# Optimization experiments

Measured on AMD Instinct MI355X. Metric: run time of the kernel, lower is better.

Reference implementation:

```python
import jax, jax.numpy as jnp
import numpy as np

B, SE, SD, IN_DIM, D, DEPTH, H, DH, M, FF, NBINS = 8, 2048, 1024, 1280, 512, 4, 8, 64, 266, 2048, 128

def _ln(x, g, b):
    mu = x.mean(-1, keepdims=True)
    var = ((x - mu) ** 2).mean(-1, keepdims=True)
    return (x - mu) / jnp.sqrt(var + 1e-5) * g + b

def _gelu(x):
    return jax.nn.gelu(x, approximate=False)

def _sinusoidal(x, dim):
    # sinusoidal embedding of integer expression bins -> [.., dim]
    half = dim // 2
    freqs = jnp.exp(-jnp.log(10000.0) * jnp.arange(half, dtype=jnp.float32) / half)
    ang = x[..., None].astype(jnp.float32) * freqs
    return jnp.concatenate([jnp.sin(ang), jnp.cos(ang)], axis=-1)

def _split_heads(x):
    b, s, _ = x.shape
    return x.reshape(b, s, H, DH).transpose(0, 2, 1, 3)

def _merge_heads(x):
    b, h, s, d = x.shape
    return x.transpose(0, 2, 1, 3).reshape(b, s, h * d)

def _favor_attention(q, k, v, proj):
    # FAVOR+ softmax-kernel linear attention (non-causal), performer-style
    dn = DH ** -0.25
    ratio = M ** -0.5
    eps = 1e-4
    qd = jnp.einsum('bhsd,md->bhsm', q * dn, proj)
    kd = jnp.einsum('bhsd,md->bhsm', k * dn, proj)
    q_diag = 0.5 * (q ** 2).sum(-1, keepdims=True) * dn * dn
    k_diag = 0.5 * (k ** 2).sum(-1, keepdims=True) * dn * dn
    qp = ratio * (jnp.exp(qd - q_diag - jnp.max(qd, axis=-1, keepdims=True)) + eps)
    kp = ratio * (jnp.exp(kd - k_diag - jnp.max(kd)) + eps)
    k_sum = kp.sum(axis=2)                                   # [b,h,m]
    d_inv = 1.0 / jnp.einsum('bhsm,bhm->bhs', qp, k_sum)     # [b,h,s]
    kv = jnp.einsum('bhsm,bhsd->bhmd', kp, v)                # [b,h,m,d]
    return jnp.einsum('bhsm,bhmd->bhsd', qp, kv) * d_inv[..., None]

def _forward(var_input_encoder, var_input_decoder, var_W, var_b, enc_ln_g, enc_ln_b, dec_ln_g, dec_ln_b, p_ln1_g, p_ln1_b, p_Wq, p_Wk, p_Wv, p_Wo, p_bo, p_ln2_g, p_ln2_b, p_w1, p_b1, p_w2, p_b2, proj, ca_Wq, ca_Wk, ca_Wv, ca_Wo, ca_bo, cross_ln_g, cross_ln_b, ffd_w1, ffd_b1, ffd_w2, ffd_b2, out_ln_g, out_ln_b, head_W, head_b, expression_encoder):
    expr = _sinusoidal(expression_encoder, D)            # [B,SE,D]
    enc = var_input_encoder @ var_W + var_b              # [B,SE,D]
    dec = var_input_decoder @ var_W + var_b              # [B,SD,D]
    x = _ln(enc + expr, enc_ln_g, enc_ln_b)
    # Performer encoder: pre-LN self-attn (FAVOR+) + pre-LN FF, residuals
    for i in range(DEPTH):
        y = _ln(x, p_ln1_g[i], p_ln1_b[i])
        q = _split_heads(y @ p_Wq[i])
        k = _split_heads(y @ p_Wk[i])
        v = _split_heads(y @ p_Wv[i])
        x = x + (_merge_heads(_favor_attention(q, k, v, proj[i])) @ p_Wo[i] + p_bo[i])
        y = _ln(x, p_ln2_g[i], p_ln2_b[i])
        x = x + (_gelu(y @ p_w1[i] + p_b1[i]) @ p_w2[i] + p_b2[i])
    context = x
    # decoder: LN -> softmax cross-attention over encoder context
    dec = _ln(dec, dec_ln_g, dec_ln_b)
    q = _split_heads(dec @ ca_Wq)
    k = _split_heads(context @ ca_Wk)
    v = _split_heads(context @ ca_Wv)
    scores = jnp.einsum('bhqd,bhkd->bhqk', q, k) * (DH ** -0.5)
    o = _merge_heads(jnp.einsum('bhqk,bhkd->bhqd', jax.nn.softmax(scores, axis=-1), v)) @ ca_Wo + ca_bo
    out = _ln(o + dec, cross_ln_g, cross_ln_b)
    out = _gelu(out @ ffd_w1 + ffd_b1) @ ffd_w2 + ffd_b2   # note: no residual around FF (as in source)
    out = _ln(out, out_ln_g, out_ln_b)
    return out @ head_W + head_b                            # [B,SD,NBINS]

def setup_inputs() -> dict:
    key = jax.random.key(0)
    ks = iter(jax.random.split(key, 64))
    def w(shape, scale=0.02):
        return jax.random.normal(next(ks), shape, dtype=jnp.float32) * scale
    inp = {
        'var_input_encoder': jax.random.normal(next(ks), (B, SE, IN_DIM), dtype=jnp.float32),
        'var_input_decoder': jax.random.normal(next(ks), (B, SD, IN_DIM), dtype=jnp.float32),
        'expression_encoder': jax.random.randint(next(ks), (B, SE), 0, NBINS, dtype=jnp.int32),
        'var_W': w((IN_DIM, D)), 'var_b': jnp.zeros((D,), jnp.float32),
        'enc_ln_g': jnp.ones((D,), jnp.float32), 'enc_ln_b': jnp.zeros((D,), jnp.float32),
        'dec_ln_g': jnp.ones((D,), jnp.float32), 'dec_ln_b': jnp.zeros((D,), jnp.float32),
        'p_ln1_g': jnp.ones((DEPTH, D), jnp.float32), 'p_ln1_b': jnp.zeros((DEPTH, D), jnp.float32),
        'p_Wq': w((DEPTH, D, H * DH)), 'p_Wk': w((DEPTH, D, H * DH)), 'p_Wv': w((DEPTH, D, H * DH)),
        'p_Wo': w((DEPTH, H * DH, D)), 'p_bo': jnp.zeros((DEPTH, D), jnp.float32),
        'p_ln2_g': jnp.ones((DEPTH, D), jnp.float32), 'p_ln2_b': jnp.zeros((DEPTH, D), jnp.float32),
        'p_w1': w((DEPTH, D, FF)), 'p_b1': jnp.zeros((DEPTH, FF), jnp.float32),
        'p_w2': w((DEPTH, FF, D)), 'p_b2': jnp.zeros((DEPTH, D), jnp.float32),
        'proj': jax.random.normal(next(ks), (DEPTH, M, DH), dtype=jnp.float32),
        'ca_Wq': w((D, H * DH)), 'ca_Wk': w((D, H * DH)), 'ca_Wv': w((D, H * DH)),
        'ca_Wo': w((H * DH, D)), 'ca_bo': jnp.zeros((D,), jnp.float32),
        'cross_ln_g': jnp.ones((D,), jnp.float32), 'cross_ln_b': jnp.zeros((D,), jnp.float32),
        'ffd_w1': w((D, FF)), 'ffd_b1': jnp.zeros((FF,), jnp.float32),
        'ffd_w2': w((FF, D)), 'ffd_b2': jnp.zeros((D,), jnp.float32),
        'out_ln_g': jnp.ones((D,), jnp.float32), 'out_ln_b': jnp.zeros((D,), jnp.float32),
        'head_W': w((D, NBINS)), 'head_b': jnp.zeros((NBINS,), jnp.float32),
    }
    return inp

def reference(var_input_encoder, var_input_decoder, expression_encoder, var_W, var_b, enc_ln_g, enc_ln_b, dec_ln_g, dec_ln_b, p_ln1_g, p_ln1_b, p_Wq, p_Wk, p_Wv, p_Wo, p_bo, p_ln2_g, p_ln2_b, p_w1, p_b1, p_w2, p_b2, proj, ca_Wq, ca_Wk, ca_Wv, ca_Wo, ca_bo, cross_ln_g, cross_ln_b, ffd_w1, ffd_b1, ffd_w2, ffd_b2, out_ln_g, out_ln_b, head_W, head_b):
    return _forward(var_input_encoder, var_input_decoder, var_W, var_b, enc_ln_g, enc_ln_b, dec_ln_g, dec_ln_b, p_ln1_g, p_ln1_b, p_Wq, p_Wk, p_Wv, p_Wo, p_bo, p_ln2_g, p_ln2_b, p_w1, p_b1, p_w2, p_b2, proj, ca_Wq, ca_Wk, ca_Wv, ca_Wo, ca_bo, cross_ln_g, cross_ln_b, ffd_w1, ffd_b1, ffd_w2, ffd_b2, out_ln_g, out_ln_b, head_W, head_b, expression_encoder)
```

## Files before the change

### kernel.cpp

```cpp
#include <hip/hip_runtime.h>
#include <hip/hip_bf16.h>
#include <math.h>

constexpr int cB = 8, cSE = 2048, cSD = 1024, cIN = 1280, cD = 512,
              cDEPTH = 4, cH = 8, cDH = 64, cM = 266, cFF = 2048, cNB = 128;
constexpr int cMP = 288;

#define DEV __device__ __forceinline__

typedef __bf16 bf16;
typedef __attribute__((ext_vector_type(8))) __bf16 bf16x8;
typedef __attribute__((ext_vector_type(4))) __bf16 bf16x4;
typedef __attribute__((ext_vector_type(2))) __bf16 bf16x2;
typedef __attribute__((ext_vector_type(4))) float f32x4;

DEV float gelu_f(float x) { return 0.5f * x * (1.0f + erff(x * 0.70710678118654752440f)); }

DEV float wave_sum(float v) {
#pragma unroll
  for (int o = 32; o; o >>= 1) v += __shfl_xor(v, o);
  return v;
}
DEV float wave_max(float v) {
#pragma unroll
  for (int o = 32; o; o >>= 1) v = fmaxf(v, __shfl_xor(v, o));
  return v;
}

#define GL2LDS(gp, lp) __builtin_amdgcn_global_load_lds(                    \
    (const __attribute__((address_space(1))) void*)(gp),                    \
    (__attribute__((address_space(3))) void*)(lp), 16, 0, 0)

template <int OUT, int ACT, bool BIAS, bool RES>
__global__ __launch_bounds__(256) void gemm_mfma(
    const bf16* __restrict__ A, const bf16* __restrict__ Bt,
    void* __restrict__ Cv, bf16* __restrict__ Cv2,
    const float* __restrict__ bias, int M, int N, int K) {
  __shared__ bf16 As[128 * 32];
  __shared__ bf16 Bs[128 * 32];
  const int t = threadIdx.x, l = t & 63, w = t >> 6;
  const int g = l >> 4, c = l & 15;
  const int nwg = gridDim.x * gridDim.y;
  int id = blockIdx.y * gridDim.x + blockIdx.x;
  if ((nwg & 7) == 0) id = (id & 7) * (nwg >> 3) + (id >> 3);
  const int m0 = (id / gridDim.x) * 128, n0 = (id % gridDim.x) * 128;
  const int wr = (w >> 1) * 64, wc = (w & 1) * 64;
  const int srow = w * 32 + (l >> 2);
  const int scol = (l & 3) * 8;
  const bf16* gA = A + (size_t)(m0 + srow) * K + scol;
  const bf16* gB = Bt + (size_t)(n0 + srow) * K + scol;
  bf16* lA = As + w * 1024;
  bf16* lB = Bs + w * 1024;

  const f32x4 zero4 = {0.f, 0.f, 0.f, 0.f};
  f32x4 acc[4][4];
#pragma unroll
  for (int i = 0; i < 4; i++)
#pragma unroll
    for (int j = 0; j < 4; j++) acc[i][j] = zero4;

  for (int k0 = 0; k0 < K; k0 += 32) {
    GL2LDS(gA + k0, lA);
    GL2LDS(gA + (size_t)16 * K + k0, lA + 512);
    GL2LDS(gB + k0, lB);
    GL2LDS(gB + (size_t)16 * K + k0, lB + 512);
    __syncthreads();
    bf16x8 af[4], bfr[4];
#pragma unroll
    for (int i = 0; i < 4; i++)
      af[i] = *(const bf16x8*)(As + (wr + i * 16 + c) * 32 + g * 8);
#pragma unroll
    for (int j = 0; j < 4; j++)
      bfr[j] = *(const bf16x8*)(Bs + (wc + j * 16 + c) * 32 + g * 8);
#pragma unroll
    for (int i = 0; i < 4; i++)
#pragma unroll
      for (int j = 0; j < 4; j++)
        acc[i][j] = __builtin_amdgcn_mfma_f32_16x16x32_bf16(af[i], bfr[j], acc[i][j], 0, 0, 0);
    __syncthreads();
  }
  float* Cf = (float*)Cv;
  bf16* Cb = (bf16*)Cv;
#pragma unroll
  for (int i = 0; i < 4; i++) {
    const int mb = m0 + wr + i * 16 + g * 4;
#pragma unroll
    for (int j = 0; j < 4; j++) {
      const int n = n0 + wc + j * 16 + c;
      const float bv = BIAS ? bias[n] : 0.f;
#pragma unroll
      for (int r = 0; r < 4; r++) {
        float v = acc[i][j][r] + bv;
        if (ACT == 1) v = gelu_f(v);
        if (ACT == 2) v *= 0.18033688011112042f;
        const size_t idx = (size_t)(mb + r) * N + n;
        if (OUT == 0 || OUT == 2) {
          float* cp = Cf + idx;
          if (RES) v += *cp;
          *cp = v;
          if (OUT == 2) Cv2[idx] = (bf16)v;
        } else {
          Cb[idx] = (bf16)v;
        }
      }
    }
  }
}

__global__ __launch_bounds__(256) void mega_prep(
    const float* __restrict__ Wq, const float* __restrict__ Wk,
    const float* __restrict__ Wv, const float* __restrict__ Wo,
    const float* __restrict__ w1, const float* __restrict__ w2,
    const float* __restrict__ var_W, const float* __restrict__ proj,
    bf16* __restrict__ WL, bf16* __restrict__ WtVar,
    bf16* __restrict__ projB4) {
  const int z = blockIdx.y, bid = blockIdx.x, t = threadIdx.x;
  if (z == 25) {
    const int idx = bid * 256 + t;
    if (idx < 4 * cMP * cDH) {
      const int layer = idx / (cMP * cDH), r = idx % (cMP * cDH);
      const int m = r >> 6;
      projB4[idx] = (bf16)(m < cM ? proj[(size_t)layer * cM * cDH + r] * 0.35355339059327373f : 0.f);
    }
    return;
  }
  __shared__ float tile[32][33];
  const float* W;
  bf16* dst;
  int K, N;
  if (z == 24) {
    W = var_W; dst = WtVar; K = 1280; N = 512;
  } else {
    const int layer = z / 6, mat = z % 6;
    bf16* base = WL + (size_t)layer * 3145728;
    if (mat < 4) {
      W = (mat == 0 ? Wq : mat == 1 ? Wk : mat == 2 ? Wv : Wo) + (size_t)layer * 262144;
      dst = base + mat * 262144; K = 512; N = 512;
    } else if (mat == 4) {
      W = w1 + (size_t)layer * 1048576; dst = base + 1048576; K = 512; N = 2048;
    } else {
      W = w2 + (size_t)layer * 1048576; dst = base + 2097152; K = 2048; N = 512;
    }
  }
  const int nt = N >> 5;
  if (bid >= nt * (K >> 5)) return;
  const int n0 = (bid % nt) * 32, k0 = (bid / nt) * 32;
  const int tx = t & 31, ty = t >> 5;
#pragma unroll
  for (int i = ty; i < 32; i += 8) tile[i][tx] = W[(size_t)(k0 + i) * N + n0 + tx];
  __syncthreads();
#pragma unroll
  for (int i = ty; i < 32; i += 8)
    dst[(size_t)(n0 + i) * K + k0 + tx] = (bf16)tile[tx][i];
}

__global__ __launch_bounds__(256) void mega_prep_dec(
    const float* __restrict__ caWq, const float* __restrict__ caWk,
    const float* __restrict__ caWv, const float* __restrict__ caWo,
    const float* __restrict__ fw1, const float* __restrict__ fw2,
    const float* __restrict__ hW, bf16* __restrict__ WD) {
  const int z = blockIdx.y, bid = blockIdx.x, t = threadIdx.x;
  __shared__ float tile[32][33];
  const float* W;
  bf16* dst;
  int K, N;
  if (z < 4) {
    W = (z == 0 ? caWq : z == 1 ? caWk : z == 2 ? caWv : caWo);
    dst = WD + z * 262144; K = 512; N = 512;
  } else if (z == 4) {
    W = fw1; dst = WD + 1048576; K = 512; N = 2048;
  } else if (z == 5) {
    W = fw2; dst = WD + 2097152; K = 2048; N = 512;
  } else {
    W = hW; dst = WD + 3145728; K = 512; N = 128;
  }
  const int nt = N >> 5;
  if (bid >= nt * (K >> 5)) return;
  const int n0 = (bid % nt) * 32, k0 = (bid / nt) * 32;
  const int tx = t & 31, ty = t >> 5;
#pragma unroll
  for (int i = ty; i < 32; i += 8) tile[i][tx] = W[(size_t)(k0 + i) * N + n0 + tx];
  __syncthreads();
#pragma unroll
  for (int i = ty; i < 32; i += 8)
    dst[(size_t)(n0 + i) * K + k0 + tx] = (bf16)tile[tx][i];
}

__global__ __launch_bounds__(256) void castf2b(
    const float* __restrict__ x, bf16* __restrict__ y, int n) {
  int i = (blockIdx.x * 256 + threadIdx.x) * 4;
  const int stride = gridDim.x * 1024;
  for (; i < n; i += stride) {
    float4 v = *(const float4*)(x + i);
    bf16x4 o;
    o[0] = (bf16)v.x; o[1] = (bf16)v.y; o[2] = (bf16)v.z; o[3] = (bf16)v.w;
    *(bf16x4*)(y + i) = o;
  }
}

__global__ __launch_bounds__(256) void vtrans(
    const bf16* __restrict__ Vh, int ld, bf16* __restrict__ Vt) {
  __shared__ bf16 tile[64][65];
  const int z = blockIdx.y, b = z >> 3, h = z & 7;
  const int s0 = blockIdx.x * 64;
  const int t = threadIdx.x;
#pragma unroll
  for (int r = t >> 3; r < 64; r += 32) {
    bf16x8 v = *(const bf16x8*)(Vh + ((size_t)b * cSE + s0 + r) * ld + h * cDH + (t & 7) * 8);
#pragma unroll
    for (int e = 0; e < 8; e++) tile[(t & 7) * 8 + e][r] = v[e];
  }
  __syncthreads();
  bf16* vz = Vt + (size_t)z * 80 * cSE;
#pragma unroll
  for (int d = t >> 3; d < 64; d += 32) {
    bf16x8 o;
#pragma unroll
    for (int e = 0; e < 8; e++) o[e] = tile[d][(t & 7) * 8 + e];
    *(bf16x8*)(vz + (size_t)d * cSE + s0 + (t & 7) * 8) = o;
  }
  const int rr = t >> 4, seg = (t & 15) * 4;
  bf16x4 ov;
  const float val = (rr == 0) ? 1.f : 0.f;
  ov[0] = (bf16)val; ov[1] = (bf16)val; ov[2] = (bf16)val; ov[3] = (bf16)val;
  *(bf16x4*)(vz + (size_t)(64 + rr) * cSE + s0 + seg) = ov;
}

__global__ __launch_bounds__(256, 1) void favor_kmax(
    const bf16* __restrict__ Kh, int ld, const bf16* __restrict__ projB,
    float* __restrict__ bmax) {
  __shared__ float sm[4];
  const int z = blockIdx.y, b = z >> 3, h = z & 7;
  const int s0 = blockIdx.x * 128;
  const int t = threadIdx.x, l = t & 63, w = t >> 6, g = l >> 4, c = l & 15;
  const int wr = (w >> 1) * 64, wcol = (w & 1) * 144;
  const f32x4 zero4 = {0.f, 0.f, 0.f, 0.f};
  f32x4 acc[4][9];
#pragma unroll
  for (int i = 0; i < 4; i++)
#pragma unroll
    for (int j = 0; j < 9; j++) acc[i][j] = zero4;
  const size_t abase = ((size_t)b * cSE + s0) * ld + h * cDH;
#pragma unroll
  for (int k0 = 0; k0 < 64; k0 += 32) {
    bf16x8 af[4];
#pragma unroll
    for (int i = 0; i < 4; i++)
      af[i] = *(const bf16x8*)(Kh + abase + (size_t)(wr + i * 16 + c) * ld + k0 + g * 8);
#pragma unroll
    for (int j = 0; j < 9; j++) {
      bf16x8 bfr = *(const bf16x8*)(projB + (wcol + j * 16 + c) * 64 + k0 + g * 8);
#pragma unroll
      for (int i = 0; i < 4; i++)
        acc[i][j] = __builtin_amdgcn_mfma_f32_16x16x32_bf16(af[i], bfr, acc[i][j], 0, 0, 0);
    }
  }
  float m = -3e38f;
#pragma unroll
  for (int i = 0; i < 4; i++)
#pragma unroll
    for (int j = 0; j < 9; j++) {
      const int mc = wcol + j * 16 + c;
      if (mc < cM) {
#pragma unroll
        for (int r = 0; r < 4; r++) m = fmaxf(m, acc[i][j][r]);
      }
    }
  m = wave_max(m);
  if (l == 0) sm[w] = m;
  __syncthreads();
  if (t == 0)
    bmax[blockIdx.y * 16 + blockIdx.x] =
        fmaxf(fmaxf(sm[0], sm[1]), fmaxf(sm[2], sm[3]));
}

__global__ __launch_bounds__(256, 1) void favor_kkv(
    const bf16* __restrict__ Kh, int ld, const bf16* __restrict__ projB,
    const bf16* __restrict__ Vt, const float* __restrict__ bmax,
    float* __restrict__ part) {
  __shared__ bf16 kp[288 * 72];
  __shared__ float sm[4];
  const int z = blockIdx.y, b = z >> 3, h = z & 7;
  const int chunk = blockIdx.x;
  const int t = threadIdx.x, l = t & 63, w = t >> 6, g = l >> 4, c = l & 15;
  float gm;
  {
    float m = -1e30f;
    for (int i = t; i < 1024; i += 256) m = fmaxf(m, bmax[i]);
    m = wave_max(m);
    if (l == 0) sm[w] = m;
    __syncthreads();
    gm = fmaxf(fmaxf(sm[0], sm[1]), fmaxf(sm[2], sm[3]));
  }
  const int pr = (w >> 1) * 32;
  const int wcol = (w & 1) * 144;
  const int wm = (w & 1) * 144, wd = (w >> 1) * 32;
  const bool dden = (wd == 32);
  const float ratio = 0.061313927f;
  const f32x4 zero4 = {0.f, 0.f, 0.f, 0.f};
  f32x4 kacc[9][2], kaccx[9];
#pragma unroll
  for (int j = 0; j < 9; j++) {
    kacc[j][0] = zero4; kacc[j][1] = zero4; kaccx[j] = zero4;
  }
  const size_t kbase = (size_t)b * cSE * ld + h * cDH;
  const size_t vtz = (size_t)z * 80 * cSE;

  for (int st = 0; st < 256; st += 64) {
    const int sg = chunk * 256 + st;
    f32x4 pacc[2][9];
#pragma unroll
    for (int i = 0; i < 2; i++)
#pragma unroll
      for (int j = 0; j < 9; j++) pacc[i][j] = zero4;
    float sq[2] = {0.f, 0.f};
#pragma unroll
    for (int k0 = 0; k0 < 64; k0 += 32) {
      bf16x8 af[2];
#pragma unroll
      for (int i = 0; i < 2; i++) {
        af[i] = *(const bf16x8*)(Kh + kbase + (size_t)(sg + pr + i * 16 + c) * ld + k0 + g * 8);
#pragma unroll
        for (int e = 0; e < 8; e++) {
          const float v = (float)af[i][e];
          sq[i] += v * v;
        }
      }
#pragma unroll
      for (int j = 0; j < 9; j++) {
        bf16x8 bfr = *(const bf16x8*)(projB + (wcol + j * 16 + c) * 64 + k0 + g * 8);
        pacc[0][j] = __builtin_amdgcn_mfma_f32_16x16x32_bf16(af[0], bfr, pacc[0][j], 0, 0, 0);
        pacc[1][j] = __builtin_amdgcn_mfma_f32_16x16x32_bf16(af[1], bfr, pacc[1][j], 0, 0, 0);
      }
    }
#pragma unroll
    for (int i = 0; i < 2; i++) {
      sq[i] += __shfl_xor(sq[i], 16);
      sq[i] += __shfl_xor(sq[i], 32);
    }
    float rowsub[2][4];
#pragma unroll
    for (int i = 0; i < 2; i++)
#pragma unroll
      for (int r = 0; r < 4; r++)
        rowsub[i][r] = gm + 0.0625f * __shfl(sq[i], g * 4 + r);
    __syncthreads();
#pragma unroll
    for (int i = 0; i < 2; i++)
#pragma unroll
      for (int j = 0; j < 9; j++) {
        const int mc = wcol + j * 16 + c;
        bf16x4 o;
#pragma unroll
        for (int r = 0; r < 4; r++) {
          const float v = (mc < cM)
              ? ratio * (__expf(pacc[i][j][r] - rowsub[i][r]) + 1e-4f) : 0.f;
          o[r] = (bf16)v;
        }
        *(bf16x4*)(kp + (size_t)mc * 72 + pr + i * 16 + g * 4) = o;
      }
    __syncthreads();
#pragma unroll
    for (int k0 = 0; k0 < 64; k0 += 32) {
      bf16x8 bv0 = *(const bf16x8*)(Vt + vtz + (size_t)(wd + c) * cSE + sg + k0 + g * 8);
      bf16x8 bv1 = *(const bf16x8*)(Vt + vtz + (size_t)(wd + 16 + c) * cSE + sg + k0 + g * 8);
      bf16x8 bvx;
      if (dden)
        bvx = *(const bf16x8*)(Vt + vtz + (size_t)(64 + c) * cSE + sg + k0 + g * 8);
#pragma unroll
      for (int j = 0; j < 9; j++) {
        bf16x8 am = *(const bf16x8*)(kp + (size_t)(wm + j * 16 + c) * 72 + k0 + g * 8);
        kacc[j][0] = __builtin_amdgcn_mfma_f32_16x16x32_bf16(am, bv0, kacc[j][0], 0, 0, 0);
        kacc[j][1] = __builtin_amdgcn_mfma_f32_16x16x32_bf16(am, bv1, kacc[j][1], 0, 0, 0);
        if (dden)
          kaccx[j] = __builtin_amdgcn_mfma_f32_16x16x32_bf16(am, bvx, kaccx[j], 0, 0, 0);
      }
    }
  }
  float* po = part + ((size_t)z * 8 + chunk) * (cMP * 80);
#pragma unroll
  for (int j = 0; j < 9; j++)
#pragma unroll
    for (int i = 0; i < 2; i++)
#pragma unroll
      for (int r = 0; r < 4; r++)
        po[(size_t)(wm + j * 16 + g * 4 + r) * 80 + wd + i * 16 + c] = kacc[j][i][r];
  if (dden) {
#pragma unroll
    for (int j = 0; j < 9; j++)
#pragma unroll
      for (int r = 0; r < 4; r++)
        po[(size_t)(wm + j * 16 + g * 4 + r) * 80 + 64 + c] = kaccx[j][r];
  }
}

__global__ __launch_bounds__(256) void kv_reduce(
    const float* __restrict__ part, bf16* __restrict__ kvT) {
  const int z = blockIdx.y, q = blockIdx.x;
  const float* p = part + (size_t)z * 8 * (cMP * 80);
  bf16* o = kvT + (size_t)z * 80 * cMP;
  const int lo = q * 5760, hi = lo + 5760;
  for (int idx = lo + threadIdx.x; idx < hi; idx += 256) {
    const int m = idx / 80, d = idx - m * 80;
    float s = 0.f;
#pragma unroll
    for (int cc = 0; cc < 8; cc++) s += p[idx + (size_t)cc * (cMP * 80)];
    o[(size_t)d * cMP + m] = (bf16)s;
  }
}

__global__ __launch_bounds__(256, 1) void favor_qout(
    const bf16* __restrict__ Qh, int ld, const bf16* __restrict__ projB,
    const bf16* __restrict__ kvT, bf16* __restrict__ Y) {
  __shared__ bf16 Plds[128 * 296];
  __shared__ float rmaxs[4][64];
  __shared__ float denl[128];
  const int z = blockIdx.y, b = z >> 3, h = z & 7;
  const int s0 = blockIdx.x * 128;
  const int t = threadIdx.x, l = t & 63, w = t >> 6, g = l >> 4, c = l & 15;
  const int wr = (w >> 1) * 64, wcol = (w & 1) * 144;
  const f32x4 zero4 = {0.f, 0.f, 0.f, 0.f};
  f32x4 acc[4][9];
#pragma unroll
  for (int i = 0; i < 4; i++)
#pragma unroll
    for (int j = 0; j < 9; j++) acc[i][j] = zero4;
  float sq[4] = {0.f, 0.f, 0.f, 0.f};
  const size_t abase = ((size_t)b * cSE + s0) * ld + h * cDH;
#pragma unroll
  for (int k0 = 0; k0 < 64; k0 += 32) {
    bf16x8 af[4];
#pragma unroll
    for (int i = 0; i < 4; i++) {
      af[i] = *(const bf16x8*)(Qh + abase + (size_t)(wr + i * 16 + c) * ld + k0 + g * 8);
#pragma unroll
      for (int e = 0; e < 8; e++) {
        const float v = (float)af[i][e];
        sq[i] += v * v;
      }
    }
#pragma unroll
    for (int j = 0; j < 9; j++) {
      bf16x8 bfr = *(const bf16x8*)(projB + (wcol + j * 16 + c) * 64 + k0 + g * 8);
#pragma unroll
      for (int i = 0; i < 4; i++)
        acc[i][j] = __builtin_amdgcn_mfma_f32_16x16x32_bf16(af[i], bfr, acc[i][j], 0, 0, 0);
    }
  }
#pragma unroll
  for (int i = 0; i < 4; i++) {
    sq[i] += __shfl_xor(sq[i], 16);
    sq[i] += __shfl_xor(sq[i], 32);
  }
  const float ratio = 0.061313927f;
  float rowsub[4][4];
#pragma unroll
  for (int i = 0; i < 4; i++)
#pragma unroll
    for (int r = 0; r < 4; r++) {
      float m = -3e38f;
#pragma unroll
      for (int j = 0; j < 9; j++) {
        const int mc = wcol + j * 16 + c;
        m = (mc < cM) ? fmaxf(m, acc[i][j][r]) : m;
      }
      m = fmaxf(m, __shfl_xor(m, 1));
      m = fmaxf(m, __shfl_xor(m, 2));
      m = fmaxf(m, __shfl_xor(m, 4));
      m = fmaxf(m, __shfl_xor(m, 8));
      rowsub[i][r] = m;
    }
  if (c == 0) {
#pragma unroll
    for (int i = 0; i < 4; i++)
#pragma unroll
      for (int r = 0; r < 4; r++) rmaxs[w][i * 16 + g * 4 + r] = rowsub[i][r];
  }
  __syncthreads();
#pragma unroll
  for (int i = 0; i < 4; i++)
#pragma unroll
    for (int r = 0; r < 4; r++) {
      const int row = i * 16 + g * 4 + r;
      rowsub[i][r] = fmaxf(rowsub[i][r], rmaxs[w ^ 1][row]) +
                     0.0625f * __shfl(sq[i], g * 4 + r);
    }
#pragma unroll
  for (int i = 0; i < 4; i++)
#pragma unroll
    for (int j = 0; j < 9; j++) {
      const int mc = wcol + j * 16 + c;
#pragma unroll
      for (int r = 0; r < 4; r++) {
        const float v = (mc < cM)
            ? ratio * (__expf(acc[i][j][r] - rowsub[i][r]) + 1e-4f) : 0.f;
        Plds[(wr + i * 16 + g * 4 + r) * 296 + mc] = (bf16)v;
      }
    }
  __syncthreads();

  const int wd = (w & 1) * 32;
  const bool dden = (wd == 32);
  f32x4 acc2[4][2], accx[4];
#pragma unroll
  for (int i = 0; i < 4; i++) {
    acc2[i][0] = zero4; acc2[i][1] = zero4; accx[i] = zero4;
  }
  const size_t kz = (size_t)z * 80 * cMP;
#pragma unroll 3
  for (int k0 = 0; k0 < cMP; k0 += 32) {
    bf16x8 bv[2], bvx;
#pragma unroll
    for (int j = 0; j < 2; j++)
      bv[j] = *(const bf16x8*)(kvT + kz + (size_t)(wd + j * 16 + c) * cMP + k0 + g * 8);
    if (dden)
      bvx = *(const bf16x8*)(kvT + kz + (size_t)(64 + c) * cMP + k0 + g * 8);
#pragma unroll
    for (int i = 0; i < 4; i++) {
      bf16x8 av = *(const bf16x8*)(Plds + (wr + i * 16 + c) * 296 + k0 + g * 8);
      acc2[i][0] = __builtin_amdgcn_mfma_f32_16x16x32_bf16(av, bv[0], acc2[i][0], 0, 0, 0);
      acc2[i][1] = __builtin_amdgcn_mfma_f32_16x16x32_bf16(av, bv[1], acc2[i][1], 0, 0, 0);
      if (dden)
        accx[i] = __builtin_amdgcn_mfma_f32_16x16x32_bf16(av, bvx, accx[i], 0, 0, 0);
    }
  }
  if (dden && c == 0) {
#pragma unroll
    for (int i = 0; i < 4; i++)
#pragma unroll
      for (int r = 0; r < 4; r++)
        denl[wr + i * 16 + g * 4 + r] = accx[i][r];
  }
  __syncthreads();
#pragma unroll
  for (int i = 0; i < 4; i++)
#pragma unroll
    for (int r = 0; r < 4; r++) {
      const int row = wr + i * 16 + g * 4 + r;
      const float inv = 1.0f / denl[row];
#pragma unroll
      for (int j = 0; j < 2; j++)
        Y[((size_t)b * cSE + s0 + row) * cD + h * cDH + wd + j * 16 + c] =
            (bf16)(acc2[i][j][r] * inv);
    }
}

template <bool ADD, bool WF, bool WB>
__global__ __launch_bounds__(256) void ln_rows(
    const float* __restrict__ in, const float* __restrict__ add,
    const float* __restrict__ g, const float* __restrict__ be,
    float* __restrict__ out, bf16* __restrict__ out2) {
  const int wid = blockIdx.x * 4 + (threadIdx.x >> 6);
  const int lane = threadIdx.x & 63;
  const float* ip = in + (size_t)wid * cD + lane * 8;
  float x[8];
  {
    float4 a = *(const float4*)ip;
    float4 b4 = *(const float4*)(ip + 4);
    x[0] = a.x; x[1] = a.y; x[2] = a.z; x[3] = a.w;
    x[4] = b4.x; x[5] = b4.y; x[6] = b4.z; x[7] = b4.w;
  }
  if (ADD) {
    const float* ap = add + (size_t)wid * cD + lane * 8;
    float4 a = *(const float4*)ap;
    float4 b4 = *(const float4*)(ap + 4);
    x[0] += a.x; x[1] += a.y; x[2] += a.z; x[3] += a.w;
    x[4] += b4.x; x[5] += b4.y; x[6] += b4.z; x[7] += b4.w;
  }
  float s = 0;
#pragma unroll
  for (int i = 0; i < 8; i++) s += x[i];
  s = wave_sum(s);
  const float mu = s * (1.0f / cD);
  float vs = 0;
#pragma unroll
  for (int i = 0; i < 8; i++) { const float d = x[i] - mu; vs += d * d; }
  vs = wave_sum(vs);
  const float rstd = 1.0f / sqrtf(vs * (1.0f / cD) + 1e-5f);
  float r[8];
#pragma unroll
  for (int i = 0; i < 8; i++) {
    const int d = lane * 8 + i;
    r[i] = (x[i] - mu) * rstd * g[d] + be[d];
  }
  if (WF) {
    float* op = out + (size_t)wid * cD + lane * 8;
    float4 a, b4;
    a.x = r[0]; a.y = r[1]; a.z = r[2]; a.w = r[3];
    b4.x = r[4]; b4.y = r[5]; b4.z = r[6]; b4.w = r[7];
    *(float4*)op = a; *(float4*)(op + 4) = b4;
  }
  if (WB) {
    bf16x8 ov;
#pragma unroll
    for (int i = 0; i < 8; i++) ov[i] = (bf16)r[i];
    *(bf16x8*)(out2 + (size_t)wid * cD + lane * 8) = ov;
  }
}

__global__ __launch_bounds__(256) void embed_ln(
    float* __restrict__ X, const int* __restrict__ ids,
    const float* __restrict__ g, const float* __restrict__ be) {
  const int wid = blockIdx.x * 4 + (threadIdx.x >> 6);
  const int lane = threadIdx.x & 63;
  const float idv = (float)ids[wid];
  float* xp = X + (size_t)wid * cD + lane * 8;
  float x[8];
  {
    float4 a = *(const float4*)xp;
    float4 b4 = *(const float4*)(xp + 4);
    x[0] = a.x; x[1] = a.y; x[2] = a.z; x[3] = a.w;
    x[4] = b4.x; x[5] = b4.y; x[6] = b4.z; x[7] = b4.w;
  }
  const float kf = -0.03597789207803197f;
#pragma unroll
  for (int i = 0; i < 8; i++) {
    const int d = lane * 8 + i;
    float e;
    if (d < 256) e = sinf(idv * expf(kf * (float)d));
    else         e = cosf(idv * expf(kf * (float)(d - 256)));
    x[i] += e;
  }
  float s = 0;
#pragma unroll
  for (int i = 0; i < 8; i++) s += x[i];
  s = wave_sum(s);
  const float mu = s * (1.0f / cD);
  float vs = 0;
#pragma unroll
  for (int i = 0; i < 8; i++) { const float d = x[i] - mu; vs += d * d; }
  vs = wave_sum(vs);
  const float rstd = 1.0f / sqrtf(vs * (1.0f / cD) + 1e-5f);
#pragma unroll
  for (int i = 0; i < 8; i++) {
    const int d = lane * 8 + i;
    xp[i] = (x[i] - mu) * rstd * g[d] + be[d];
  }
}

__global__ __launch_bounds__(256) void flash_mfma(
    const bf16* __restrict__ Q, const bf16* __restrict__ Kc,
    const bf16* __restrict__ Vc, bf16* __restrict__ O, int ldkv) {
  __shared__ __align__(16) bf16 KP[4 * 16 * 136];
  __shared__ __align__(16) bf16 Vs[80 * 136];
  const int id = blockIdx.x;
  const int b = (id & 63) >> 3, h = id & 7, qb = id >> 6;
  const int t = threadIdx.x, l = t & 63, w = t >> 6, g = l >> 4, c = l & 15;
  const int q0 = qb * 64 + w * 16;
  bf16x8 aq[2];
  {
    const bf16* qp = Q + ((size_t)b * cSD + q0 + c) * cD + h * cDH + g * 8;
    aq[0] = *(const bf16x8*)qp;
    aq[1] = *(const bf16x8*)(qp + 32);
  }
  for (int idx = t; idx < 16 * 136; idx += 256) {
    const int rr = idx / 136, cc = idx - rr * 136;
    Vs[(64 + rr) * 136 + cc] = (bf16)(rr == 0 ? 1.f : 0.f);
  }
  const f32x4 zero4 = {0.f, 0.f, 0.f, 0.f};
  f32x4 o5[5];
#pragma unroll
  for (int j = 0; j < 5; j++) o5[j] = zero4;
  float mrow[4];
#pragma unroll
  for (int r = 0; r < 4; r++) mrow[r] = -1e30f;

  const int kr = t >> 1, kof = (t & 1) * 32;
  const int sidx = t & 31, dseg = t >> 5;
  const size_t kvbase = (size_t)b * cSE * ldkv + h * cDH;
  char* KsC = (char*)KP;
  bf16* Pw = KP + w * 16 * 136;
  const float T2 = 11.541560327111708f;

  bf16x8 pk[4], pv[4];
  auto LOADR = [&](int kt) {
    const bf16* kp = Kc + kvbase + (size_t)(kt + kr) * ldkv + kof;
#pragma unroll
    for (int i = 0; i < 4; i++) pk[i] = *(const bf16x8*)(kp + i * 8);
    const bf16* vp = Vc + kvbase + (size_t)(kt + 4 * sidx) * ldkv + dseg * 8;
#pragma unroll
    for (int i = 0; i < 4; i++) pv[i] = *(const bf16x8*)(vp + (size_t)i * ldkv);
  };
  auto WRITEL = [&]() {
    const int sw = (kr & 7) << 4;
#pragma unroll
    for (int i = 0; i < 4; i++)
      *(bf16x8*)(KsC + kr * 128 + (((kof + i * 8) * 2) ^ sw)) = pk[i];
#pragma unroll
    for (int e = 0; e < 8; e++) {
      bf16x4 q4;
      q4[0] = pv[0][e]; q4[1] = pv[1][e]; q4[2] = pv[2][e]; q4[3] = pv[3][e];
      *(bf16x4*)(Vs + (dseg * 8 + e) * 136 + 4 * sidx) = q4;
    }
  };
  LOADR(0);
  WRITEL();

  for (int kt = 0; kt < cSE; kt += 128) {
    const bool more = (kt + 128 < cSE);
    if (more) LOADR(kt + 128);
    __syncthreads();
    f32x4 s4[8];
#pragma unroll
    for (int t2 = 0; t2 < 8; t2++) {
      const int kr2 = t2 * 16 + c;
      const int sw2 = (kr2 & 7) << 4;
      bf16x8 bk0 = *(const bf16x8*)(KsC + kr2 * 128 + ((g * 16) ^ sw2));
      bf16x8 bk1 = *(const bf16x8*)(KsC + kr2 * 128 + ((64 + g * 16) ^ sw2));
      f32x4 z = zero4;
      z = __builtin_amdgcn_mfma_f32_16x16x32_bf16(aq[0], bk0, z, 0, 0, 0);
      z = __builtin_amdgcn_mfma_f32_16x16x32_bf16(aq[1], bk1, z, 0, 0, 0);
      s4[t2] = z;
    }
    __syncthreads();
#pragma unroll
    for (int r = 0; r < 4; r++) {
      float xv[8];
#pragma unroll
      for (int t2 = 0; t2 < 8; t2++) xv[t2] = s4[t2][r];
      float tm = xv[0];
#pragma unroll
      for (int t2 = 1; t2 < 8; t2++) tm = fmaxf(tm, xv[t2]);
      tm = fmaxf(tm, __shfl_xor(tm, 1));
      tm = fmaxf(tm, __shfl_xor(tm, 2));
      tm = fmaxf(tm, __shfl_xor(tm, 4));
      tm = fmaxf(tm, __shfl_xor(tm, 8));
      if (tm > mrow[r] + T2) {
        const float corr = exp2f(mrow[r] - tm);
        mrow[r] = tm;
#pragma unroll
        for (int j = 0; j < 5; j++) o5[j][r] *= corr;
      }
      const float m = mrow[r];
      const int qr = g * 4 + r;
#pragma unroll
      for (int t2 = 0; t2 < 8; t2++)
        Pw[qr * 136 + t2 * 16 + c] = (bf16)exp2f(xv[t2] - m);
    }
    bf16x8 pa[4];
#pragma unroll
    for (int ks = 0; ks < 4; ks++)
      pa[ks] = *(const bf16x8*)(Pw + c * 136 + ks * 32 + g * 8);
#pragma unroll
    for (int j = 0; j < 5; j++) {
#pragma unroll
      for (int ks = 0; ks < 4; ks++) {
        bf16x8 bv = *(const bf16x8*)(Vs + (j * 16 + c) * 136 + ks * 32 + g * 8);
        o5[j] = __builtin_amdgcn_mfma_f32_16x16x32_bf16(pa[ks], bv, o5[j], 0, 0, 0);
      }
    }
    __syncthreads();
    if (more) WRITEL();
  }
#pragma unroll
  for (int r = 0; r < 4; r++) {
    const float den = __shfl(o5[4][r], l & 48);
    const float inv = 1.0f / den;
    const size_t row = (size_t)b * cSD + q0 + g * 4 + r;
#pragma unroll
    for (int j = 0; j < 4; j++)
      O[row * cD + h * cDH + j * 16 + c] = (bf16)(o5[j][r] * inv);
  }
}

extern "C" void kernel_launch(void* const* d_in, const int* in_sizes, int n_in,
                              void* d_out, int out_size, void* d_ws, size_t ws_size,
                              hipStream_t stream) {
  const float* in_enc = (const float*)d_in[0];
  const float* in_dec = (const float*)d_in[1];
  const int* expr = (const int*)d_in[2];
  const float* var_W = (const float*)d_in[3];
  const float* var_b = (const float*)d_in[4];
  const float* enc_g = (const float*)d_in[5];
  const float* enc_b = (const float*)d_in[6];
  const float* dec_g = (const float*)d_in[7];
  const float* dec_b = (const float*)d_in[8];
  const float* ln1_g = (const float*)d_in[9];
  const float* ln1_b = (const float*)d_in[10];
  const float* Wq = (const float*)d_in[11];
  const float* Wk = (const float*)d_in[12];
  const float* Wv = (const float*)d_in[13];
  const float* Wo = (const float*)d_in[14];
  const float* bo = (const float*)d_in[15];
  const float* ln2_g = (const float*)d_in[16];
  const float* ln2_b = (const float*)d_in[17];
  const float* w1 = (const float*)d_in[18];
  const float* b1 = (const float*)d_in[19];
  const float* w2 = (const float*)d_in[20];
  const float* b2 = (const float*)d_in[21];
  const float* proj = (const float*)d_in[22];
  const float* caWq = (const float*)d_in[23];
  const float* caWk = (const float*)d_in[24];
  const float* caWv = (const float*)d_in[25];
  const float* caWo = (const float*)d_in[26];
  const float* cabo = (const float*)d_in[27];
  const float* crg = (const float*)d_in[28];
  const float* crb = (const float*)d_in[29];
  const float* fw1 = (const float*)d_in[30];
  const float* fb1 = (const float*)d_in[31];
  const float* fw2 = (const float*)d_in[32];
  const float* fb2 = (const float*)d_in[33];
  const float* og = (const float*)d_in[34];
  const float* ob = (const float*)d_in[35];
  const float* hW = (const float*)d_in[36];
  const float* hb = (const float*)d_in[37];

  float* X     = (float*)d_ws;
  float* DC    = X + 8388608;
  bf16*  QKV   = (bf16*)(DC + 4194304);
  bf16*  Vt    = QKV + 25165824;
  bf16*  Pb    = Vt + 10485760;
  float* part  = (float*)(Pb + 50331648);
  bf16*  kvT   = (bf16*)(part + 11796480);
  float* bmax  = (float*)(kvT + 1474560);
  bf16*  Yb    = (bf16*)(bmax + 1040);
  bf16*  DCb   = Yb + 8388608;
  bf16*  Wt    = DCb + 4194304;
  bf16*  projB4 = Wt + 1048576;
  const size_t need_bytes = (size_t)75458576 * 4;
  if (ws_size < need_bytes) return;

  bf16* encB = Pb;
  bf16* decB = (bf16*)part;
  bf16* Pmid = Pb;
  bf16* WL   = Pb + 33554432;
  bf16* Xb   = Vt;
  bf16* Qc   = Pb + 8388608;
  bf16* KVc  = Pb + 12582912;
  bf16* Fb   = Pb + 29360128;
  bf16* Pm2  = Pb + 33554432;
  bf16* WD   = (bf16*)part;

  const dim3 blk(256);

  castf2b<<<2048, blk, 0, stream>>>(in_enc, encB, 16384 * 1280);
  castf2b<<<2048, blk, 0, stream>>>(in_dec, decB, 8192 * 1280);
  mega_prep<<<dim3(1024, 26), blk, 0, stream>>>(Wq, Wk, Wv, Wo, w1, w2, var_W, proj,
                                                WL, Wt, projB4);
  gemm_mfma<0, 0, true, false><<<dim3(4, 128), blk, 0, stream>>>(encB, Wt, X, nullptr, var_b, 16384, 512, 1280);
  gemm_mfma<0, 0, true, false><<<dim3(4, 64), blk, 0, stream>>>(decB, Wt, DC, nullptr, var_b, 8192, 512, 1280);
  embed_ln<<<4096, blk, 0, stream>>>(X, expr, enc_g, enc_b);
  ln_rows<false, true, true><<<2048, blk, 0, stream>>>(DC, nullptr, dec_g, dec_b, DC, DCb);

  for (int i = 0; i < cDEPTH; i++) {
    bf16* Wl = WL + (size_t)i * 3145728;
    bf16* projB = projB4 + (size_t)i * (cMP * cDH);
    ln_rows<false, false, true><<<4096, blk, 0, stream>>>(X, nullptr, ln1_g + i * cD, ln1_b + i * cD, nullptr, Yb);
    gemm_mfma<1, 0, false, false><<<dim3(12, 128), blk, 0, stream>>>(Yb, Wl, QKV, nullptr, nullptr, 16384, 1536, 512);
    vtrans<<<dim3(32, 64), blk, 0, stream>>>(QKV + 1024, 1536, Vt);
    favor_kmax<<<dim3(16, 64), blk, 0, stream>>>(QKV + 512, 1536, projB, bmax);
    favor_kkv<<<dim3(8, 64), blk, 0, stream>>>(QKV + 512, 1536, projB, Vt, bmax, part);
    kv_reduce<<<dim3(4, 64), blk, 0, stream>>>(part, kvT);
    favor_qout<<<dim3(16, 64), blk, 0, stream>>>(QKV, 1536, projB, kvT, Yb);
    gemm_mfma<0, 0, true, true><<<dim3(4, 128), blk, 0, stream>>>(Yb, Wl + 786432, X, nullptr, bo + i * cD, 16384, 512, 512);
    ln_rows<false, false, true><<<4096, blk, 0, stream>>>(X, nullptr, ln2_g + i * cD, ln2_b + i * cD, nullptr, Yb);
    gemm_mfma<1, 1, true, false><<<dim3(16, 128), blk, 0, stream>>>(Yb, Wl + 1048576, Pmid, nullptr, b1 + i * cFF, 16384, 2048, 512);
    if (i < cDEPTH - 1) {
      gemm_mfma<0, 0, true, true><<<dim3(4, 128), blk, 0, stream>>>(Pmid, Wl + 2097152, X, nullptr, b2 + i * cD, 16384, 512, 2048);
    } else {
      gemm_mfma<2, 0, true, true><<<dim3(4, 128), blk, 0, stream>>>(Pmid, Wl + 2097152, X, Xb, b2 + i * cD, 16384, 512, 2048);
    }
  }

  mega_prep_dec<<<dim3(1024, 7), blk, 0, stream>>>(caWq, caWk, caWv, caWo, fw1, fw2, hW, WD);
  gemm_mfma<1, 2, false, false><<<dim3(4, 64), blk, 0, stream>>>(DCb, WD, Qc, nullptr, nullptr, 8192, 512, 512);
  gemm_mfma<1, 0, false, false><<<dim3(8, 128), blk, 0, stream>>>(Xb, WD + 262144, KVc, nullptr, nullptr, 16384, 1024, 512);
  flash_mfma<<<dim3(1024), blk, 0, stream>>>(Qc, KVc, KVc + 512, Fb, 1024);
  gemm_mfma<0, 0, true, false><<<dim3(4, 64), blk, 0, stream>>>(Fb, WD + 786432, X, nullptr, cabo, 8192, 512, 512);
  ln_rows<true, false, true><<<2048, blk, 0, stream>>>(X, DC, crg, crb, nullptr, Yb);
  gemm_mfma<1, 1, true, false><<<dim3(16, 64), blk, 0, stream>>>(Yb, WD + 1048576, Pm2, nullptr, fb1, 8192, 2048, 512);
  gemm_mfma<0, 0, true, false><<<dim3(4, 64), blk, 0, stream>>>(Pm2, WD + 2097152, X + 4194304, nullptr, fb2, 8192, 512, 2048);
  ln_rows<false, false, true><<<2048, blk, 0, stream>>>(X + 4194304, nullptr, og, ob, nullptr, Yb);
  gemm_mfma<0, 0, true, false><<<dim3(1, 64), blk, 0, stream>>>(Yb, WD + 3145728, (float*)d_out, nullptr, hb, 8192, 128, 512);
}
```

Baseline: 1.977 ms.

## Process K=64 per GEMM step and merge small prep kernels into fewer launches

The GEMM main loop now loads two 32-wide K slices per barrier pair into doubled LDS buffers, halving the number of __syncthreads per tile. The input float-to-bf16 casts are folded into the mega_prep launch as extra grid rows. The V transpose and K-max kernels are merged into one favor_prep launch. These remove launch and barrier overhead, at the cost of more LDS per GEMM block (reducing occupancy) and a heavier kmax branch whose launch_bounds minimum-blocks hint is dropped.

```diff
diff --git a/kernel.cpp b/kernel.cpp
--- a/kernel.cpp
+++ b/kernel.cpp
@@ -36,8 +36,8 @@
     const bf16* __restrict__ A, const bf16* __restrict__ Bt,
     void* __restrict__ Cv, bf16* __restrict__ Cv2,
     const float* __restrict__ bias, int M, int N, int K) {
-  __shared__ bf16 As[128 * 32];
-  __shared__ bf16 Bs[128 * 32];
+  __shared__ bf16 As[2 * 128 * 32];
+  __shared__ bf16 Bs[2 * 128 * 32];
   const int t = threadIdx.x, l = t & 63, w = t >> 6;
   const int g = l >> 4, c = l & 15;
   const int nwg = gridDim.x * gridDim.y;
@@ -59,24 +59,31 @@
 #pragma unroll
     for (int j = 0; j < 4; j++) acc[i][j] = zero4;
 
-  for (int k0 = 0; k0 < K; k0 += 32) {
+  for (int k0 = 0; k0 < K; k0 += 64) {
     GL2LDS(gA + k0, lA);
     GL2LDS(gA + (size_t)16 * K + k0, lA + 512);
     GL2LDS(gB + k0, lB);
     GL2LDS(gB + (size_t)16 * K + k0, lB + 512);
+    GL2LDS(gA + k0 + 32, lA + 4096);
+    GL2LDS(gA + (size_t)16 * K + k0 + 32, lA + 4096 + 512);
+    GL2LDS(gB + k0 + 32, lB + 4096);
+    GL2LDS(gB + (size_t)16 * K + k0 + 32, lB + 4096 + 512);
     __syncthreads();
-    bf16x8 af[4], bfr[4];
-#pragma unroll
-    for (int i = 0; i < 4; i++)
-      af[i] = *(const bf16x8*)(As + (wr + i * 16 + c) * 32 + g * 8);
-#pragma unroll
-    for (int j = 0; j < 4; j++)
-      bfr[j] = *(const bf16x8*)(Bs + (wc + j * 16 + c) * 32 + g * 8);
-#pragma unroll
-    for (int i = 0; i < 4; i++)
+#pragma unroll
+    for (int hh = 0; hh < 2; hh++) {
+      bf16x8 af[4], bfr[4];
+#pragma unroll
+      for (int i = 0; i < 4; i++)
+        af[i] = *(const bf16x8*)(As + hh * 4096 + (wr + i * 16 + c) * 32 + g * 8);
 #pragma unroll
       for (int j = 0; j < 4; j++)
-        acc[i][j] = __builtin_amdgcn_mfma_f32_16x16x32_bf16(af[i], bfr[j], acc[i][j], 0, 0, 0);
+        bfr[j] = *(const bf16x8*)(Bs + hh * 4096 + (wc + j * 16 + c) * 32 + g * 8);
+#pragma unroll
+      for (int i = 0; i < 4; i++)
+#pragma unroll
+        for (int j = 0; j < 4; j++)
+          acc[i][j] = __builtin_amdgcn_mfma_f32_16x16x32_bf16(af[i], bfr[j], acc[i][j], 0, 0, 0);
+    }
     __syncthreads();
   }
   float* Cf = (float*)Cv;
@@ -112,9 +119,25 @@
     const float* __restrict__ Wv, const float* __restrict__ Wo,
     const float* __restrict__ w1, const float* __restrict__ w2,
     const float* __restrict__ var_W, const float* __restrict__ proj,
+    const float* __restrict__ in_enc, const float* __restrict__ in_dec,
     bf16* __restrict__ WL, bf16* __restrict__ WtVar,
-    bf16* __restrict__ projB4) {
+    bf16* __restrict__ projB4, bf16* __restrict__ encB,
+    bf16* __restrict__ decB) {
   const int z = blockIdx.y, bid = blockIdx.x, t = threadIdx.x;
+  if (z >= 26) {
+    const float* src = (z == 26) ? in_enc : in_dec;
+    bf16* dst = (z == 26) ? encB : decB;
+    const int n = (z == 26) ? 16384 * 1280 : 8192 * 1280;
+    int i = (bid * 256 + t) * 4;
+    const int stride = 1024 * 256 * 4;
+    for (; i < n; i += stride) {
+      float4 v = *(const float4*)(src + i);
+      bf16x4 o;
+      o[0] = (bf16)v.x; o[1] = (bf16)v.y; o[2] = (bf16)v.z; o[3] = (bf16)v.w;
+      *(bf16x4*)(dst + i) = o;
+    }
+    return;
+  }
   if (z == 25) {
     const int idx = bid * 256 + t;
     if (idx < 4 * cMP * cDH) {
@@ -186,53 +209,43 @@
     dst[(size_t)(n0 + i) * K + k0 + tx] = (bf16)tile[tx][i];
 }
 
-__global__ __launch_bounds__(256) void castf2b(
-    const float* __restrict__ x, bf16* __restrict__ y, int n) {
-  int i = (blockIdx.x * 256 + threadIdx.x) * 4;
-  const int stride = gridDim.x * 1024;
-  for (; i < n; i += stride) {
-    float4 v = *(const float4*)(x + i);
-    bf16x4 o;
-    o[0] = (bf16)v.x; o[1] = (bf16)v.y; o[2] = (bf16)v.z; o[3] = (bf16)v.w;
-    *(bf16x4*)(y + i) = o;
-  }
-}
-
-__global__ __launch_bounds__(256) void vtrans(
-    const bf16* __restrict__ Vh, int ld, bf16* __restrict__ Vt) {
-  __shared__ bf16 tile[64][65];
+__global__ __launch_bounds__(256) void favor_prep(
+    const bf16* __restrict__ QKV, const bf16* __restrict__ projB,
+    bf16* __restrict__ Vt, float* __restrict__ bmax) {
   const int z = blockIdx.y, b = z >> 3, h = z & 7;
-  const int s0 = blockIdx.x * 64;
   const int t = threadIdx.x;
-#pragma unroll
-  for (int r = t >> 3; r < 64; r += 32) {
-    bf16x8 v = *(const bf16x8*)(Vh + ((size_t)b * cSE + s0 + r) * ld + h * cDH + (t & 7) * 8);
-#pragma unroll
-    for (int e = 0; e < 8; e++) tile[(t & 7) * 8 + e][r] = v[e];
-  }
-  __syncthreads();
-  bf16* vz = Vt + (size_t)z * 80 * cSE;
-#pragma unroll
-  for (int d = t >> 3; d < 64; d += 32) {
-    bf16x8 o;
-#pragma unroll
-    for (int e = 0; e < 8; e++) o[e] = tile[d][(t & 7) * 8 + e];
-    *(bf16x8*)(vz + (size_t)d * cSE + s0 + (t & 7) * 8) = o;
-  }
-  const int rr = t >> 4, seg = (t & 15) * 4;
-  bf16x4 ov;
-  const float val = (rr == 0) ? 1.f : 0.f;
-  ov[0] = (bf16)val; ov[1] = (bf16)val; ov[2] = (bf16)val; ov[3] = (bf16)val;
-  *(bf16x4*)(vz + (size_t)(64 + rr) * cSE + s0 + seg) = ov;
-}
-
-__global__ __launch_bounds__(256, 1) void favor_kmax(
-    const bf16* __restrict__ Kh, int ld, const bf16* __restrict__ projB,
-    float* __restrict__ bmax) {
+  const int ld = 1536;
+  if (blockIdx.x < 32) {
+    __shared__ bf16 tile[64][65];
+    const bf16* Vh = QKV + 1024;
+    const int s0 = blockIdx.x * 64;
+#pragma unroll
+    for (int r = t >> 3; r < 64; r += 32) {
+      bf16x8 v = *(const bf16x8*)(Vh + ((size_t)b * cSE + s0 + r) * ld + h * cDH + (t & 7) * 8);
+#pragma unroll
+      for (int e = 0; e < 8; e++) tile[(t & 7) * 8 + e][r] = v[e];
+    }
+    __syncthreads();
+    bf16* vz = Vt + (size_t)z * 80 * cSE;
+#pragma unroll
+    for (int d = t >> 3; d < 64; d += 32) {
+      bf16x8 o;
+#pragma unroll
+      for (int e = 0; e < 8; e++) o[e] = tile[d][(t & 7) * 8 + e];
+      *(bf16x8*)(vz + (size_t)d * cSE + s0 + (t & 7) * 8) = o;
+    }
+    const int rr = t >> 4, seg = (t & 15) * 4;
+    bf16x4 ov;
+    const float val = (rr == 0) ? 1.f : 0.f;
+    ov[0] = (bf16)val; ov[1] = (bf16)val; ov[2] = (bf16)val; ov[3] = (bf16)val;
+    *(bf16x4*)(vz + (size_t)(64 + rr) * cSE + s0 + seg) = ov;
+    return;
+  }
   __shared__ float sm[4];
-  const int z = blockIdx.y, b = z >> 3, h = z & 7;
-  const int s0 = blockIdx.x * 128;
-  const int t = threadIdx.x, l = t & 63, w = t >> 6, g = l >> 4, c = l & 15;
+  const bf16* Kh = QKV + 512;
+  const int xb = blockIdx.x - 32;
+  const int s0 = xb * 128;
+  const int l = t & 63, w = t >> 6, g = l >> 4, c = l & 15;
   const int wr = (w >> 1) * 64, wcol = (w & 1) * 144;
   const f32x4 zero4 = {0.f, 0.f, 0.f, 0.f};
   f32x4 acc[4][9];
@@ -270,8 +283,7 @@
   if (l == 0) sm[w] = m;
   __syncthreads();
   if (t == 0)
-    bmax[blockIdx.y * 16 + blockIdx.x] =
-        fmaxf(fmaxf(sm[0], sm[1]), fmaxf(sm[2], sm[3]));
+    bmax[z * 16 + xb] = fmaxf(fmaxf(sm[0], sm[1]), fmaxf(sm[2], sm[3]));
 }
 
 __global__ __launch_bounds__(256, 1) void favor_kkv(
@@ -833,10 +845,9 @@
 
   const dim3 blk(256);
 
-  castf2b<<<2048, blk, 0, stream>>>(in_enc, encB, 16384 * 1280);
-  castf2b<<<2048, blk, 0, stream>>>(in_dec, decB, 8192 * 1280);
-  mega_prep<<<dim3(1024, 26), blk, 0, stream>>>(Wq, Wk, Wv, Wo, w1, w2, var_W, proj,
-                                                WL, Wt, projB4);
+  mega_prep<<<dim3(1024, 28), blk, 0, stream>>>(Wq, Wk, Wv, Wo, w1, w2, var_W, proj,
+                                                in_enc, in_dec, WL, Wt, projB4,
+                                                encB, decB);
   gemm_mfma<0, 0, true, false><<<dim3(4, 128), blk, 0, stream>>>(encB, Wt, X, nullptr, var_b, 16384, 512, 1280);
   gemm_mfma<0, 0, true, false><<<dim3(4, 64), blk, 0, stream>>>(decB, Wt, DC, nullptr, var_b, 8192, 512, 1280);
   embed_ln<<<4096, blk, 0, stream>>>(X, expr, enc_g, enc_b);
@@ -847,8 +858,7 @@
     bf16* projB = projB4 + (size_t)i * (cMP * cDH);
     ln_rows<false, false, true><<<4096, blk, 0, stream>>>(X, nullptr, ln1_g + i * cD, ln1_b + i * cD, nullptr, Yb);
     gemm_mfma<1, 0, false, false><<<dim3(12, 128), blk, 0, stream>>>(Yb, Wl, QKV, nullptr, nullptr, 16384, 1536, 512);
-    vtrans<<<dim3(32, 64), blk, 0, stream>>>(QKV + 1024, 1536, Vt);
-    favor_kmax<<<dim3(16, 64), blk, 0, stream>>>(QKV + 512, 1536, projB, bmax);
+    favor_prep<<<dim3(48, 64), blk, 0, stream>>>(QKV, projB, Vt, bmax);
     favor_kkv<<<dim3(8, 64), blk, 0, stream>>>(QKV + 512, 1536, projB, Vt, bmax, part);
     kv_reduce<<<dim3(4, 64), blk, 0, stream>>>(part, kvT);
     favor_qout<<<dim3(16, 64), blk, 0, stream>>>(QKV, 1536, projB, kvT, Yb);
```

Result: faster. 1.932 ms (-2.3%).
